# Optimization experiments

Hardware: AMD Instinct MI355X
Metric: run time of the kernel (lower is better)

Reference implementation:

```python
import jax, jax.numpy as jnp
import numpy as np

EMBED_DIM = 1024

def setup_inputs() -> dict:
    key = jax.random.key(0)
    kx, kwq, kbq, kwk, kbk, kwv, kbv = jax.random.split(key, 7)
    d = EMBED_DIM
    s = 1.0 / np.sqrt(d)
    x = jax.random.normal(kx, (4, 2048, d), dtype=jnp.float32)
    # nn.Linear weights are [out, in]; we store transposed [in, out] for x @ W
    Wq = jax.random.uniform(kwq, (d, d), jnp.float32, -s, s)
    bq = jax.random.uniform(kbq, (d,), jnp.float32, -s, s)
    Wk = jax.random.uniform(kwk, (d, d), jnp.float32, -s, s)
    bk = jax.random.uniform(kbk, (d,), jnp.float32, -s, s)
    Wv = jax.random.uniform(kwv, (d, d), jnp.float32, -s, s)
    bv = jax.random.uniform(kbv, (d,), jnp.float32, -s, s)
    return {"x": x, "Wq": Wq, "bq": bq, "Wk": Wk, "bk": bk, "Wv": Wv, "bv": bv}

def reference(x, Wq, bq, Wk, bk, Wv, bv):
    d = x.shape[-1]
    q = x @ Wq + bq            # [B, S, D]
    k = x @ Wk + bk            # [B, S, D]
    v = x @ Wv + bv            # [B, S, D]
    scores = jnp.einsum('bsd,btd->bst', q, k) / jnp.sqrt(jnp.asarray(d, x.dtype))
    attn = jax.nn.softmax(scores, axis=-1)  # [B, S, S]
    return jnp.einsum('bst,btd->bsd', attn, v)
```

## Files before the change

### kernel.cpp

```cpp
#include <hip/hip_runtime.h>
#include <hip/hip_bf16.h>
#include <stdint.h>


typedef short bf16x8 __attribute__((ext_vector_type(8)));
typedef float f32x4 __attribute__((ext_vector_type(4)));
typedef unsigned short us4 __attribute__((ext_vector_type(4)));
typedef _Float16 h4 __attribute__((ext_vector_type(4)));
typedef unsigned short us;

#define B_ 4
#define S_ 2048
#define D_ 1024

__device__ __forceinline__ us f2bf(float f) {
  unsigned int u = __float_as_uint(f);
  unsigned int r = (u + 0x7fffu + ((u >> 16) & 1u)) >> 16;
  return (us)r;
}

__device__ __forceinline__ void gl2lds16(void* lds, const void* g) {
  __builtin_amdgcn_global_load_lds(
      (const __attribute__((address_space(1))) unsigned int*)(uintptr_t)g,
      (__attribute__((address_space(3))) unsigned int*)(uintptr_t)lds,
      16, 0, 0);
}

__device__ __forceinline__ void sched_fence() { __builtin_amdgcn_sched_barrier(0); }
__device__ __forceinline__ void barrier_f() {
  sched_fence(); __builtin_amdgcn_s_barrier(); sched_fence();
}

template<int EPI>
__global__ __launch_bounds__(512, 2) void gemm256(
    const us* __restrict__ Aall, const us* __restrict__ Ball,
    size_t aBatch, size_t bBatch, int sAe, int sBe, int nt,
    const float* __restrict__ bq, const float* __restrict__ bk,
    const float* __restrict__ bv, void* __restrict__ outp,
    us* __restrict__ vtb) {
  __shared__ __align__(16) us lds[5 * 16384];
  const int tid = threadIdx.x, lane = tid & 63, wave = tid >> 6;
  const int wm = wave >> 2, wn = wave & 3;
  const int m0 = blockIdx.x * 256, n0 = blockIdx.y * 256;
  const size_t bz = blockIdx.z;
  const char* gA = (const char*)(Aall + bz * aBatch + (size_t)m0 * sAe);
  const char* gB = (const char*)(Ball + bz * bBatch + (size_t)n0 * sBe);
  const size_t sA = (size_t)sAe * 2, sB = (size_t)sBe * 2;

  const int r15 = lane & 15, kg = lane >> 4;
  const int srcslot = ((lane & 7) ^ (lane >> 3)) << 4;
  const int ldl = lane >> 3;
  const int brow = (wn & 1) * 64;
  const int nh = 2 * nt;

  auto stage = [&](int h, int c) {
    char* dst = (char*)lds + (h % 5) * 32768 +
                (c < 2 ? c * 8192 : 16384 + (c - 2) * 8192) + wave * 1024;
    int row = (h & 1) * 128 + (c < 2 ? c * 64 : (c - 2) * 64) + wave * 8 + ldl;
    const char* src = (c < 2 ? gA + (size_t)row * sA : gB + (size_t)row * sB) +
                      (size_t)(h >> 1) * 128 + srcslot;
    gl2lds16(dst, src);
  };

#pragma unroll
  for (int h = 0; h < 3; ++h)
#pragma unroll
    for (int c = 0; c < 4; ++c) stage(h, c);
  asm volatile("s_waitcnt vmcnt(4)" ::: "memory");
  barrier_f();

  f32x4 acc[8][4] = {};
  for (int t = 0; t < nt; ++t) {
    const char* hbA = (const char*)lds + ((2 * t + wm) % 5) * 32768;
    const char* hbB = (const char*)lds + ((2 * t + (wn >> 1)) % 5) * 32768 + 16384;
    const int hs_base = 2 * t + 3;
    bf16x8 Br[4];
#pragma unroll
    for (int p = 0; p < 4; ++p) {
      const int kh = p >> 1, mq = p & 1;
      bf16x8 Ar[4];
#pragma unroll
      for (int f = 0; f < 4; ++f) {
        int lr = (mq * 4 + f) * 16 + r15;
        Ar[f] = *(const bf16x8*)(hbA + lr * 128 +
                                 ((((kh << 2) | kg) ^ (lr & 7)) << 4));
      }
      if (mq == 0) {
#pragma unroll
        for (int n = 0; n < 4; ++n) {
          int lr = brow + n * 16 + r15;
          Br[n] = *(const bf16x8*)(hbB + lr * 128 +
                                   ((((kh << 2) | kg) ^ (lr & 7)) << 4));
        }
      }
      {
        int cp = p * 2;
        int h1 = hs_base + (cp >> 2);
        if (h1 < nh) stage(h1, cp & 3);
        int h2 = hs_base + ((cp + 1) >> 2);
        if (h2 < nh) stage(h2, (cp + 1) & 3);
      }
      barrier_f();
      __builtin_amdgcn_s_setprio(1);
#pragma unroll
      for (int n = 0; n < 4; ++n)
#pragma unroll
        for (int f = 0; f < 4; ++f)
          acc[mq * 4 + f][n] = __builtin_amdgcn_mfma_f32_16x16x32_bf16(
              Ar[f], Br[n], acc[mq * 4 + f][n], 0, 0, 0);
      __builtin_amdgcn_s_setprio(0);
      if (p == 3) {
        if (t <= nt - 3) asm volatile("s_waitcnt vmcnt(4)" ::: "memory");
        else             asm volatile("s_waitcnt vmcnt(0)" ::: "memory");
      }
      barrier_f();
    }
  }

#pragma unroll
  for (int fm = 0; fm < 8; ++fm)
#pragma unroll
    for (int fn = 0; fn < 4; ++fn) {
      int col = n0 + wn * 64 + fn * 16 + r15;
      int row0 = m0 + wm * 128 + fm * 16 + ((lane >> 4) << 2);
      if constexpr (EPI == 0) {
        int mat = col >> 10;
        const float* bp = (mat == 0) ? bq : (mat == 1) ? bk : bv;
        float bb = bp[col & 1023];
        if (mat < 2) {
          us* ob = (us*)outp + ((size_t)mat << 23);
#pragma unroll
          for (int r = 0; r < 4; ++r)
            ob[(size_t)(row0 + r) * D_ + (col & 1023)] = f2bf(acc[fm][fn][r] + bb);
        } else {
          int b = row0 >> 11, trow = row0 & 2047, dcol = col & 1023;
          us4 v4 = {f2bf(acc[fm][fn][0] + bb), f2bf(acc[fm][fn][1] + bb),
                    f2bf(acc[fm][fn][2] + bb), f2bf(acc[fm][fn][3] + bb)};
          *(us4*)(vtb + (size_t)b * D_ * S_ + (size_t)dcol * S_ + trow) = v4;
        }
      } else {
        _Float16* sc = (_Float16*)outp + bz * (size_t)(S_ * S_);
#pragma unroll
        for (int r = 0; r < 4; ++r)
          sc[(size_t)(row0 + r) * S_ + col] = (_Float16)(acc[fm][fn][r] * 0.03125f);
      }
    }
}

template<int BM, int R0, int R1>
__device__ __forceinline__ void stageR(us* buf, const us* gA, size_t sA,
                                       const us* gB, size_t sB,
                                       int wave, int lane) {
  int slot = ((lane & 7) ^ (lane >> 3)) << 4;
  char* l = (char*)buf;
#pragma unroll
  for (int r = R0; r < R1; ++r) {
    int row = r * 64 + wave * 8 + (lane >> 3);
    const char* src;
    if (r * 64 < BM)
      src = (const char*)gA + (size_t)row * sA + slot;
    else
      src = (const char*)gB + (size_t)(row - BM) * sB + slot;
    gl2lds16(l + r * 8192 + wave * 1024, src);
  }
}

template<int EPI, int BM, int BN, int WMS, int WNS>
__global__ __launch_bounds__(512, 2) void gemm8p(
    const us* __restrict__ Aall, const us* __restrict__ Ball,
    size_t aBatch, size_t bBatch, int sAe, int sBe, int nt,
    void* __restrict__ outp) {
  __shared__ __align__(16) us lds[3][(BM + BN) * 64];
  int tid = threadIdx.x, lane = tid & 63, wave = tid >> 6;
  int wm = wave / WNS, wn = wave % WNS;
  int m0 = blockIdx.x * BM, n0 = blockIdx.y * BN;
  size_t bz = blockIdx.z;
  const us* gA = Aall + bz * aBatch + (size_t)m0 * sAe;
  const us* gB = Ball + bz * bBatch + (size_t)n0 * sBe;
  size_t sA = (size_t)sAe * 2, sB = (size_t)sBe * 2;

  stageR<BM, 0, 6>(lds[0], gA, sA, gB, sB, wave, lane);
  stageR<BM, 0, 6>(lds[1], gA + 64, sA, gB + 64, sB, wave, lane);

  int r15 = lane & 15, kg = lane >> 4, l7 = lane & 7;
  int x0 = (kg ^ l7) << 4;
  f32x4 acc[4][4] = {};

  for (int t = 0; t < nt; ++t) {
    if (t == nt - 1) asm volatile("s_waitcnt vmcnt(0)" ::: "memory");
    else             asm volatile("s_waitcnt vmcnt(6)" ::: "memory");
    barrier_f();
    const us* buf = lds[t % 3];
    us* nbuf = (us*)lds[(t + 2) % 3];
    bool dostage = (t + 2 < nt);
    const us* gA2 = gA + (size_t)(t + 2) * 64;
    const us* gB2 = gB + (size_t)(t + 2) * 64;
    const char* pa = (const char*)buf + (size_t)(wm * 64 + r15) * 128;
    const char* pb = (const char*)buf + (size_t)(BM + wn * 64 + r15) * 128;

    if (dostage) stageR<BM, 0, 3>(nbuf, gA2, sA, gB2, sB, wave, lane);
    bf16x8 A0[4], B0[4];
#pragma unroll
    for (int f = 0; f < 4; ++f) A0[f] = *(const bf16x8*)(pa + f * 2048 + x0);
#pragma unroll
    for (int f = 0; f < 4; ++f) B0[f] = *(const bf16x8*)(pb + f * 2048 + x0);
    __builtin_amdgcn_s_setprio(1);
#pragma unroll
    for (int fn = 0; fn < 4; ++fn)
#pragma unroll
      for (int fm = 0; fm < 4; ++fm)
        acc[fm][fn] = __builtin_amdgcn_mfma_f32_16x16x32_bf16(A0[fm], B0[fn], acc[fm][fn], 0, 0, 0);
    __builtin_amdgcn_s_setprio(0);

    if (dostage) stageR<BM, 3, 6>(nbuf, gA2, sA, gB2, sB, wave, lane);
    bf16x8 A1[4], B1[4];
#pragma unroll
    for (int f = 0; f < 4; ++f) A1[f] = *(const bf16x8*)(pa + f * 2048 + (x0 ^ 64));
#pragma unroll
    for (int f = 0; f < 4; ++f) B1[f] = *(const bf16x8*)(pb + f * 2048 + (x0 ^ 64));
    __builtin_amdgcn_s_setprio(1);
#pragma unroll
    for (int fn = 0; fn < 4; ++fn)
#pragma unroll
      for (int fm = 0; fm < 4; ++fm)
        acc[fm][fn] = __builtin_amdgcn_mfma_f32_16x16x32_bf16(A1[fm], B1[fn], acc[fm][fn], 0, 0, 0);
    __builtin_amdgcn_s_setprio(0);
  }

#pragma unroll
  for (int fm = 0; fm < 4; ++fm)
#pragma unroll
    for (int fn = 0; fn < 4; ++fn) {
      int col = n0 + wn * 64 + fn * 16 + r15;
      int row0 = m0 + wm * 64 + fm * 16 + ((lane >> 4) << 2);
      float* ob = (float*)outp + bz * (size_t)(S_ * D_);
#pragma unroll
      for (int r = 0; r < 4; ++r)
        ob[(size_t)(row0 + r) * D_ + col] = acc[fm][fn][r];
    }
}

__global__ __launch_bounds__(256) void wt_prep(const float* __restrict__ Wq,
                                               const float* __restrict__ Wk,
                                               const float* __restrict__ Wv,
                                               us* __restrict__ wtb) {
  __shared__ us hs[64][65];
  int mat = blockIdx.z;
  const float* W = (mat == 0) ? Wq : (mat == 1) ? Wk : Wv;
  int n0 = blockIdx.x * 64, k0 = blockIdx.y * 64;
  int tid = threadIdx.x;
#pragma unroll
  for (int i = 0; i < 16; ++i) {
    int idx = tid + i * 256;
    int r = idx >> 6, c = idx & 63;
    hs[r][c] = f2bf(W[(size_t)(k0 + r) * D_ + (n0 + c)]);
  }
  __syncthreads();
  us* o = wtb + ((size_t)mat << 20);
#pragma unroll
  for (int i = 0; i < 16; ++i) {
    int idx = tid + i * 256;
    int r = idx >> 6, c = idx & 63;
    o[(size_t)(n0 + r) * D_ + (k0 + c)] = hs[c][r];
  }
}

__global__ __launch_bounds__(256) void xcast(const float* __restrict__ x,
                                             us* __restrict__ xb) {
  size_t i = ((size_t)blockIdx.x * 256 + threadIdx.x) * 8;
  float4 f0 = *(const float4*)(x + i);
  float4 f1 = *(const float4*)(x + i + 4);
  float vals[8] = {f0.x, f0.y, f0.z, f0.w, f1.x, f1.y, f1.z, f1.w};
  union { bf16x8 v; us s_[8]; } H;
#pragma unroll
  for (int e = 0; e < 8; ++e) H.s_[e] = f2bf(vals[e]);
  *(bf16x8*)(xb + i) = H.v;
}

__global__ __launch_bounds__(256) void softmax_k(const _Float16* __restrict__ scores,
                                                 us* __restrict__ pb) {
  int row = blockIdx.x, tid = threadIdx.x, lane = tid & 63, wave = tid >> 6;
  const _Float16* s = scores + (size_t)row * S_;
  h4 a4 = ((const h4*)s)[tid];
  h4 b4 = ((const h4*)s)[256 + tid];
  float a[8] = {(float)a4.x, (float)a4.y, (float)a4.z, (float)a4.w,
                (float)b4.x, (float)b4.y, (float)b4.z, (float)b4.w};
  float m = a[0];
#pragma unroll
  for (int e = 1; e < 8; ++e) m = fmaxf(m, a[e]);
#pragma unroll
  for (int o = 32; o; o >>= 1) m = fmaxf(m, __shfl_xor(m, o));
  __shared__ float red[4];
  if (lane == 0) red[wave] = m;
  __syncthreads();
  m = fmaxf(fmaxf(red[0], red[1]), fmaxf(red[2], red[3]));
  float p[8];
  float sum = 0.f;
#pragma unroll
  for (int e = 0; e < 8; ++e) { p[e] = expf(a[e] - m); sum += p[e]; }
#pragma unroll
  for (int o = 32; o; o >>= 1) sum += __shfl_xor(sum, o);
  __syncthreads();
  if (lane == 0) red[wave] = sum;
  __syncthreads();
  float inv = 1.0f / (red[0] + red[1] + red[2] + red[3]);
  us h[8];
#pragma unroll
  for (int e = 0; e < 8; ++e) h[e] = f2bf(p[e] * inv);
  size_t base = (size_t)row * S_;
  *(us4*)(pb + base + tid * 4) = (us4){h[0], h[1], h[2], h[3]};
  *(us4*)(pb + base + 1024 + tid * 4) = (us4){h[4], h[5], h[6], h[7]};
}

extern "C" void kernel_launch(void* const* d_in, const int* in_sizes, int n_in,
                              void* d_out, int out_size, void* d_ws, size_t ws_size,
                              hipStream_t stream) {
  const float* x  = (const float*)d_in[0];
  const float* Wq = (const float*)d_in[1];
  const float* bq = (const float*)d_in[2];
  const float* Wk = (const float*)d_in[3];
  const float* bk = (const float*)d_in[4];
  const float* Wv = (const float*)d_in[5];
  const float* bv = (const float*)d_in[6];
  float* out = (float*)d_out;
  char* ws = (char*)d_ws;
  const size_t MB = 1024 * 1024;
  us* qb   = (us*)(ws + 0 * MB);
  us* vtb  = (us*)(ws + 32 * MB);
  us* wtb  = (us*)(ws + 48 * MB);
  us* xb   = (us*)(ws + 54 * MB);
  _Float16* scores = (_Float16*)(ws + 70 * MB);
  us* pb   = (us*)(ws + 102 * MB);
  us* kb   = (us*)(ws + 16 * MB);

  wt_prep<<<dim3(16, 16, 3), 256, 0, stream>>>(Wq, Wk, Wv, wtb);
  xcast<<<dim3(4096), 256, 0, stream>>>(x, xb);
  gemm256<0><<<dim3(32, 12, 1), 512, 0, stream>>>(
      xb, wtb, 0, 0, D_, D_, 16, bq, bk, bv, qb, vtb);
  gemm256<1><<<dim3(8, 8, 4), 512, 0, stream>>>(
      qb, kb, (size_t)S_ * D_, (size_t)S_ * D_, D_, D_, 16,
      nullptr, nullptr, nullptr, scores, nullptr);
  softmax_k<<<dim3(B_ * S_), 256, 0, stream>>>(scores, pb);
  gemm8p<2, 256, 128, 4, 2><<<dim3(8, 8, 4), 512, 0, stream>>>(
      pb, vtb, (size_t)S_ * S_, (size_t)D_ * S_, S_, S_, 32, out);
}
```

Baseline: 169.9 us.

## Rewrite 256x256 GEMM mainloop as triple-buffered K=32 stages with one barrier

Replaces the five-slot half-tile LDS ring with its interleaved staging and two barriers per sub-step by a simple three-buffer pipeline. Each iteration now covers K=32, loads all A and B fragments at once and issues 32 MFMAs after a single barrier. The LDS swizzle is changed to match the 64-byte row pitch. The aim is less barrier and scheduling overhead per MFMA, at the cost of a shallower prefetch depth and more loop iterations (nt doubled to 32).

New measurement: 165.1 us. 1.03x faster.

```diff
diff --git a/kernel.cpp b/kernel.cpp
--- a/kernel.cpp
+++ b/kernel.cpp
@@ -32,13 +32,13 @@
 }
 
 template<int EPI>
-__global__ __launch_bounds__(512, 2) void gemm256(
+__global__ __launch_bounds__(512, 2) void gemm256k(
     const us* __restrict__ Aall, const us* __restrict__ Ball,
     size_t aBatch, size_t bBatch, int sAe, int sBe, int nt,
     const float* __restrict__ bq, const float* __restrict__ bk,
     const float* __restrict__ bv, void* __restrict__ outp,
     us* __restrict__ vtb) {
-  __shared__ __align__(16) us lds[5 * 16384];
+  __shared__ __align__(16) us lds3[3][16384];
   const int tid = threadIdx.x, lane = tid & 63, wave = tid >> 6;
   const int wm = wave >> 2, wn = wave & 3;
   const int m0 = blockIdx.x * 256, n0 = blockIdx.y * 256;
@@ -48,73 +48,51 @@
   const size_t sA = (size_t)sAe * 2, sB = (size_t)sBe * 2;
 
   const int r15 = lane & 15, kg = lane >> 4;
-  const int srcslot = ((lane & 7) ^ (lane >> 3)) << 4;
-  const int ldl = lane >> 3;
-  const int brow = (wn & 1) * 64;
-  const int nh = 2 * nt;
-
-  auto stage = [&](int h, int c) {
-    char* dst = (char*)lds + (h % 5) * 32768 +
-                (c < 2 ? c * 8192 : 16384 + (c - 2) * 8192) + wave * 1024;
-    int row = (h & 1) * 128 + (c < 2 ? c * 64 : (c - 2) * 64) + wave * 8 + ldl;
-    const char* src = (c < 2 ? gA + (size_t)row * sA : gB + (size_t)row * sB) +
-                      (size_t)(h >> 1) * 128 + srcslot;
-    gl2lds16(dst, src);
+  const int srcslot = (((lane & 3) ^ ((lane >> 3) & 3)) << 4);
+  const int srow = wave * 16 + (lane >> 2);
+
+  auto stage = [&](int bi, int t) {
+    char* l = (char*)lds3[bi];
+    const size_t koff = (size_t)t * 64;
+#pragma unroll
+    for (int r = 0; r < 4; ++r) {
+      int row = r * 128 + srow;
+      const char* src = (row < 256)
+          ? gA + (size_t)row * sA + koff + srcslot
+          : gB + (size_t)(row - 256) * sB + koff + srcslot;
+      gl2lds16(l + r * 8192 + wave * 1024, src);
+    }
   };
 
-#pragma unroll
-  for (int h = 0; h < 3; ++h)
-#pragma unroll
-    for (int c = 0; c < 4; ++c) stage(h, c);
-  asm volatile("s_waitcnt vmcnt(4)" ::: "memory");
-  barrier_f();
+  stage(0, 0);
+  stage(1, 1);
 
   f32x4 acc[8][4] = {};
   for (int t = 0; t < nt; ++t) {
-    const char* hbA = (const char*)lds + ((2 * t + wm) % 5) * 32768;
-    const char* hbB = (const char*)lds + ((2 * t + (wn >> 1)) % 5) * 32768 + 16384;
-    const int hs_base = 2 * t + 3;
-    bf16x8 Br[4];
-#pragma unroll
-    for (int p = 0; p < 4; ++p) {
-      const int kh = p >> 1, mq = p & 1;
-      bf16x8 Ar[4];
-#pragma unroll
-      for (int f = 0; f < 4; ++f) {
-        int lr = (mq * 4 + f) * 16 + r15;
-        Ar[f] = *(const bf16x8*)(hbA + lr * 128 +
-                                 ((((kh << 2) | kg) ^ (lr & 7)) << 4));
-      }
-      if (mq == 0) {
-#pragma unroll
-        for (int n = 0; n < 4; ++n) {
-          int lr = brow + n * 16 + r15;
-          Br[n] = *(const bf16x8*)(hbB + lr * 128 +
-                                   ((((kh << 2) | kg) ^ (lr & 7)) << 4));
-        }
-      }
-      {
-        int cp = p * 2;
-        int h1 = hs_base + (cp >> 2);
-        if (h1 < nh) stage(h1, cp & 3);
-        int h2 = hs_base + ((cp + 1) >> 2);
-        if (h2 < nh) stage(h2, (cp + 1) & 3);
-      }
-      barrier_f();
-      __builtin_amdgcn_s_setprio(1);
-#pragma unroll
-      for (int n = 0; n < 4; ++n)
-#pragma unroll
-        for (int f = 0; f < 4; ++f)
-          acc[mq * 4 + f][n] = __builtin_amdgcn_mfma_f32_16x16x32_bf16(
-              Ar[f], Br[n], acc[mq * 4 + f][n], 0, 0, 0);
-      __builtin_amdgcn_s_setprio(0);
-      if (p == 3) {
-        if (t <= nt - 3) asm volatile("s_waitcnt vmcnt(4)" ::: "memory");
-        else             asm volatile("s_waitcnt vmcnt(0)" ::: "memory");
-      }
-      barrier_f();
-    }
+    if (t == nt - 1) asm volatile("s_waitcnt vmcnt(0)" ::: "memory");
+    else             asm volatile("s_waitcnt vmcnt(4)" ::: "memory");
+    barrier_f();
+    if (t + 2 < nt) stage((t + 2) % 3, t + 2);
+    const char* buf = (const char*)lds3[t % 3];
+
+    bf16x8 Af[8], Bf[4];
+#pragma unroll
+    for (int f = 0; f < 8; ++f) {
+      int tr = wm * 128 + f * 16 + r15;
+      Af[f] = *(const bf16x8*)(buf + tr * 64 + ((kg ^ ((tr >> 1) & 3)) << 4));
+    }
+#pragma unroll
+    for (int n = 0; n < 4; ++n) {
+      int tr = 256 + wn * 64 + n * 16 + r15;
+      Bf[n] = *(const bf16x8*)(buf + tr * 64 + ((kg ^ ((tr >> 1) & 3)) << 4));
+    }
+    __builtin_amdgcn_s_setprio(1);
+#pragma unroll
+    for (int n = 0; n < 4; ++n)
+#pragma unroll
+      for (int f = 0; f < 8; ++f)
+        acc[f][n] = __builtin_amdgcn_mfma_f32_16x16x32_bf16(Af[f], Bf[n], acc[f][n], 0, 0, 0);
+    __builtin_amdgcn_s_setprio(0);
   }
 
 #pragma unroll
@@ -326,19 +304,19 @@
   char* ws = (char*)d_ws;
   const size_t MB = 1024 * 1024;
   us* qb   = (us*)(ws + 0 * MB);
+  us* kb   = (us*)(ws + 16 * MB);
   us* vtb  = (us*)(ws + 32 * MB);
   us* wtb  = (us*)(ws + 48 * MB);
   us* xb   = (us*)(ws + 54 * MB);
   _Float16* scores = (_Float16*)(ws + 70 * MB);
   us* pb   = (us*)(ws + 102 * MB);
-  us* kb   = (us*)(ws + 16 * MB);
 
   wt_prep<<<dim3(16, 16, 3), 256, 0, stream>>>(Wq, Wk, Wv, wtb);
   xcast<<<dim3(4096), 256, 0, stream>>>(x, xb);
-  gemm256<0><<<dim3(32, 12, 1), 512, 0, stream>>>(
-      xb, wtb, 0, 0, D_, D_, 16, bq, bk, bv, qb, vtb);
-  gemm256<1><<<dim3(8, 8, 4), 512, 0, stream>>>(
-      qb, kb, (size_t)S_ * D_, (size_t)S_ * D_, D_, D_, 16,
+  gemm256k<0><<<dim3(32, 12, 1), 512, 0, stream>>>(
+      xb, wtb, 0, 0, D_, D_, 32, bq, bk, bv, qb, vtb);
+  gemm256k<1><<<dim3(8, 8, 4), 512, 0, stream>>>(
+      qb, kb, (size_t)S_ * D_, (size_t)S_ * D_, D_, D_, 32,
       nullptr, nullptr, nullptr, scores, nullptr);
   softmax_k<<<dim3(B_ * S_), 256, 0, stream>>>(scores, pb);
   gemm8p<2, 256, 128, 4, 2><<<dim3(8, 8, 4), 512, 0, stream>>>(
```
